# Optimization experiments

Hardware: AMD Instinct MI355X
Metric: run time of the kernel (lower is better)

## Reference

```python
import math
import jax, jax.numpy as jnp
import numpy as np

H = 256      # hidden_size
HEADS = 8
DK = H // HEADS
B = 32
DL = 290     # drug length
PL = 1000    # protein length


def _pe(length, d):
    # sinusoidal positional encoding, d even
    pos = jnp.arange(length, dtype=jnp.float32)[:, None]
    div = jnp.exp(jnp.arange(0, d, 2, dtype=jnp.float32) * (-math.log(10000.0) / d))
    ang = pos * div  # [L, d/2]
    pe = jnp.zeros((length, d), jnp.float32)
    pe = pe.at[:, 0::2].set(jnp.sin(ang)).at[:, 1::2].set(jnp.cos(ang))
    return pe


def setup_inputs() -> dict:
    key = jax.random.key(0)
    ks = iter(jax.random.split(key, 48))
    def lin(din, dout):
        return jax.random.normal(next(ks), (din, dout), jnp.float32) * 0.02, jnp.zeros((dout,), jnp.float32)
    inp = {}
    inp['drug'] = jax.random.normal(next(ks), (B, DL, H), jnp.float32)
    inp['protein'] = jax.random.normal(next(ks), (B, PL, H), jnp.float32)
    inp['scale_d'] = jnp.ones((1,), jnp.float32)
    inp['scale_p'] = jnp.ones((1,), jnp.float32)
    for name in ['q_d', 'k_p', 'v_p', 'q_p', 'k_d', 'v_d', 'out_d', 'out_p']:
        w, b = lin(H, H)
        inp['w_' + name] = w
        inp['b_' + name] = b
    inp['alpha'] = jnp.asarray(0.5, jnp.float32)
    for name in ['fc_dp', 'fc_pd']:
        w, b = lin(HEADS, H)
        inp['w_' + name] = w
        inp['b_' + name] = b
    for name in ['gd', 'gp']:
        w, b = lin(H, H)
        inp['w_' + name] = w
        inp['b_' + name] = b
    return inp


def _split_heads(x):
    b, l, _ = x.shape
    return x.reshape(b, l, HEADS, DK).transpose(0, 2, 1, 3)  # [b, h, l, dk]


def _forward(drug, protein, scale_d, scale_p,
             w_q_d, b_q_d, w_k_p, b_k_p, w_v_p, b_v_p,
             w_q_p, b_q_p, w_k_d, b_k_d, w_v_d, b_v_d,
             alpha, w_out_d, b_out_d, w_out_p, b_out_p,
             w_fc_dp, b_fc_dp, w_fc_pd, b_fc_pd,
             w_gd, b_gd, w_gp, b_gp):
    b, dl, h = drug.shape
    pl = protein.shape[1]
    # positional encoding (buffers, non-learned except scale)
    drug_e = drug + scale_d * _pe(dl, h)
    prot_e = protein + scale_p * _pe(pl, h)

    Qd = _split_heads(drug_e @ w_q_d + b_q_d)   # [b,h,dl,dk]
    Kp = _split_heads(prot_e @ w_k_p + b_k_p)   # [b,h,pl,dk]
    Vp = _split_heads(prot_e @ w_v_p + b_v_p)
    Qp = _split_heads(prot_e @ w_q_p + b_q_p)
    Kd = _split_heads(drug_e @ w_k_d + b_k_d)
    Vd = _split_heads(drug_e @ w_v_d + b_v_d)

    inv_sqrt = 1.0 / math.sqrt(DK)
    attn_dp = jnp.einsum('bhid,bhjd->bhij', Qd, Kp) * inv_sqrt      # [b,h,dl,pl]
    # (Q_p K_d^T)^T along last two dims -> [b,h,dl,pl]
    attn_pd = jnp.einsum('bhjd,bhid->bhij', Qp, Kd) * inv_sqrt
    a = jax.nn.sigmoid(alpha)
    A = jax.nn.softmax(a * attn_dp + (1.0 - a) * attn_pd, axis=-1)  # [b,h,dl,pl]

    ctx_d = jnp.einsum('bhij,bhjd->bhid', A, Vp)  # [b,h,dl,dk]
    ctx_p = jnp.einsum('bhij,bhid->bhjd', A, Vd)  # [b,h,pl,dk]
    ctx_d = ctx_d.transpose(0, 2, 1, 3).reshape(b, dl, h) @ w_out_d + b_out_d
    ctx_p = ctx_p.transpose(0, 2, 1, 3).reshape(b, pl, h) @ w_out_p + b_out_p

    attn_dp_m = jnp.mean(A, axis=-1).transpose(0, 2, 1)   # [b,dl,heads]
    drug_attn = attn_dp_m @ w_fc_dp + b_fc_dp             # [b,dl,h]
    attn_pd_m = jnp.mean(A, axis=-2).transpose(0, 2, 1)   # [b,pl,heads]
    prot_attn = attn_pd_m @ w_fc_pd + b_fc_pd             # [b,pl,h]

    drug_gate = jax.nn.sigmoid(drug_e @ w_gd + b_gd)
    prot_gate = jax.nn.sigmoid(prot_e @ w_gp + b_gp)
    ctx_d = ctx_d * drug_gate
    ctx_p = ctx_p * prot_gate

    drug_upd = drug_e + ctx_d * jax.nn.sigmoid(drug_attn)
    prot_upd = prot_e + ctx_p * jax.nn.sigmoid(prot_attn)
    return jnp.concatenate([drug_upd, prot_upd], axis=1)  # [b, dl+pl, h]


def reference(drug, protein, scale_d, scale_p,
              w_q_d, b_q_d, w_k_p, b_k_p, w_v_p, b_v_p,
              w_q_p, b_q_p, w_k_d, b_k_d, w_v_d, b_v_d,
              alpha, w_out_d, b_out_d, w_out_p, b_out_p,
              w_fc_dp, b_fc_dp, w_fc_pd, b_fc_pd,
              w_gd, b_gd, w_gp, b_gp):
    return _forward(drug, protein, scale_d, scale_p,
                    w_q_d, b_q_d, w_k_p, b_k_p, w_v_p, b_v_p,
                    w_q_p, b_q_p, w_k_d, b_k_d, w_v_d, b_v_d,
                    alpha, w_out_d, b_out_d, w_out_p, b_out_p,
                    w_fc_dp, b_fc_dp, w_fc_pd, b_fc_pd,
                    w_gd, b_gd, w_gp, b_gp)
```

## Files before the change

kernel.cpp:

```cpp
#include <hip/hip_runtime.h>
#include <math.h>

typedef __attribute__((ext_vector_type(8))) short bf16x8;
typedef __attribute__((ext_vector_type(4))) float f32x4;
typedef unsigned short u16;
typedef unsigned int u32;

#define DEVFN static __device__ __forceinline__

constexpr int NB  = 32;
constexpr int DLn = 290;
constexpr int PLc = 1000;
constexpr int MD  = NB * DLn;
constexpr int MP  = NB * PLc;
constexpr int NS2 = 323;
constexpr int SP2 = 73;
constexpr int SG2 = 41;

DEVFN u16 f2b(float f) {
    u32 u = __builtin_bit_cast(u32, f);
    u32 r = u + 0x7fffu + ((u >> 16) & 1u);
    return (u16)(r >> 16);
}
DEVFN u16 f2bh(float f) { __bf16 h = (__bf16)f; return __builtin_bit_cast(u16, h); }
DEVFN float b2f(u16 s) { return __builtin_bit_cast(float, (u32)s << 16); }
DEVFN float sigm(float x) { return 1.0f / (1.0f + __expf(-x)); }
DEVFN float fexp2(float x) { return __builtin_amdgcn_exp2f(x); }
DEVFN int sw(int row, int col, int stride) { return row * stride + (col ^ ((row & 7) << 3)); }

__global__ void pe_kernel(float* __restrict__ pe) {
    int p = blockIdx.x, c = threadIdx.x;
    float div = __expf((float)(c & ~1) * (-9.210340371976184f / 256.0f));
    float ang = (float)p * div;
    pe[p * 256 + c] = (c & 1) ? cosf(ang) : sinf(ang);
}

__global__ void fcprep_kernel(const float* __restrict__ w, const float* __restrict__ b,
                              float* __restrict__ dfc) {
    int c = threadIdx.x;
    float s = b[c];
    #pragma unroll
    for (int hh = 0; hh < 8; hh++) s += 0.001f * w[hh * 256 + c];
    dfc[c] = s;
}

__global__ __launch_bounds__(256) void eadd_kernel(
        const float* __restrict__ drug, const float* __restrict__ prot,
        const float* __restrict__ scale_d, const float* __restrict__ scale_p,
        const float* __restrict__ pe,
        u16* __restrict__ e_d, u16* __restrict__ e_p) {
    int idx = blockIdx.x * 256 + threadIdx.x;
    int r = idx >> 6, c4 = (idx & 63) * 4;
    if (r < MD) {
        int i = r % DLn;
        float s = scale_d[0];
        float4 dv = *(const float4*)&drug[(size_t)r * 256 + c4];
        float4 pv = *(const float4*)&pe[i * 256 + c4];
        u16 o[4];
        o[0] = f2b(dv.x + s * pv.x); o[1] = f2b(dv.y + s * pv.y);
        o[2] = f2b(dv.z + s * pv.z); o[3] = f2b(dv.w + s * pv.w);
        *(uint2*)&e_d[(size_t)r * 256 + c4] = *(uint2*)o;
    } else {
        int rr = r - MD;
        int j = rr % PLc;
        float s = scale_p[0];
        float4 dv = *(const float4*)&prot[(size_t)rr * 256 + c4];
        float4 pv = *(const float4*)&pe[j * 256 + c4];
        u16 o[4];
        o[0] = f2b(dv.x + s * pv.x); o[1] = f2b(dv.y + s * pv.y);
        o[2] = f2b(dv.z + s * pv.z); o[3] = f2b(dv.w + s * pv.w);
        *(uint2*)&e_p[(size_t)rr * 256 + c4] = *(uint2*)o;
    }
}

struct WPtrs { const float* w[10]; };
__global__ __launch_bounds__(256) void wprep_kernel(WPtrs wp, u16* __restrict__ wt) {
    __shared__ u16 t[64][66];
    int m = blockIdx.y, tile = blockIdx.x;
    int k0 = (tile >> 2) * 64, n0 = (tile & 3) * 64;
    const float* w = wp.w[m];
    int r = threadIdx.x >> 6, c = threadIdx.x & 63;
    #pragma unroll
    for (int q = 0; q < 16; q++) {
        int rr = r + q * 4;
        t[rr][c] = f2b(w[(size_t)(k0 + rr) * 256 + n0 + c]);
    }
    __syncthreads();
    #pragma unroll
    for (int q = 0; q < 16; q++) {
        int rr = r + q * 4;
        wt[((size_t)m << 16) + (size_t)(n0 + rr) * 256 + k0 + c] = t[c][rr];
    }
}

struct PM { const u16* BT; const float* bias; u16* C; int sig; };
struct PCfg {
    const u16* Ab;
    PM m[4];
};
struct PCfg2 {
    PCfg c0, c1;
    const float* x0; const float* x1;
    const u16* gate0; const u16* gate1;
    const float* cm;
    const float* dfc;
    const float* wfc1; const float* bfc1;
    const float* scale0; const float* scale1;
    const float* pe;
    float* out;
};

template<int NM>
__global__ __launch_bounds__(512) void proj_kernel(PCfg2 cfgs) {
    const int d = blockIdx.x;
    const int x = d & 7, q = d >> 3;
    const int u  = (NM == 4) ? (q & 15) : (q & 3);
    const int sg = (NM == 4) ? (q >> 4) : (q >> 2);
    const int s = sg * 8 + x;
    if (s >= NS2) return;
    const int mi = (NM == 4) ? (u >> 2) : 0;
    const int nt = (NM == 4) ? (u & 3) : u;
    const bool f1 = s < SP2;
    const int mt = f1 ? s : s - SP2;
    const int Mrows = f1 ? MD : MP;

    const u16* Ab   = f1 ? cfgs.c0.Ab : cfgs.c1.Ab;
    const u16*   BT   = f1 ? (mi==0?cfgs.c0.m[0].BT  :mi==1?cfgs.c0.m[1].BT  :mi==2?cfgs.c0.m[2].BT  :cfgs.c0.m[3].BT)
                           : (mi==0?cfgs.c1.m[0].BT  :mi==1?cfgs.c1.m[1].BT  :mi==2?cfgs.c1.m[2].BT  :cfgs.c1.m[3].BT);
    const float* bias = f1 ? (mi==0?cfgs.c0.m[0].bias:mi==1?cfgs.c0.m[1].bias:mi==2?cfgs.c0.m[2].bias:cfgs.c0.m[3].bias)
                           : (mi==0?cfgs.c1.m[0].bias:mi==1?cfgs.c1.m[1].bias:mi==2?cfgs.c1.m[2].bias:cfgs.c1.m[3].bias);
    u16*         C    = f1 ? (mi==0?cfgs.c0.m[0].C   :mi==1?cfgs.c0.m[1].C   :mi==2?cfgs.c0.m[2].C   :cfgs.c0.m[3].C)
                           : (mi==0?cfgs.c1.m[0].C   :mi==1?cfgs.c1.m[1].C   :mi==2?cfgs.c1.m[2].C   :cfgs.c1.m[3].C);
    const int    sig  = f1 ? (mi==0?cfgs.c0.m[0].sig :mi==1?cfgs.c0.m[1].sig :mi==2?cfgs.c0.m[2].sig :cfgs.c0.m[3].sig)
                           : (mi==0?cfgs.c1.m[0].sig :mi==1?cfgs.c1.m[1].sig :mi==2?cfgs.c1.m[2].sig :cfgs.c1.m[3].sig);

    __shared__ u16 Bs[64 * 256];
    __shared__ float fcb[(NM == 1) ? 2304 : 4];
    const int tid = threadIdx.x;
    const int lane = tid & 63, w = tid >> 6, ln = lane & 15, g = lane >> 4;

    const int gc = tid & 31;
    const int rb = (tid >> 5) * 4;
    uint4 bv[4];
    #pragma unroll
    for (int kk = 0; kk < 4; kk++) {
        const int r = rb + kk;
        const int nur = ((r >> 5) & 1) * 32 + ((r >> 2) & 3) * 8 + ((r >> 4) & 1) * 4 + (r & 3);
        bv[kk] = *(const uint4*)(BT + (size_t)(nt * 64 + nur) * 256 + gc * 8);
    }

    const int row = mt * 128 + w * 16 + ln;
    const bool rowok = row < Mrows;
    bf16x8 Af[8];
    if (rowok) {
        const u16* Ap = Ab + (size_t)row * 256 + g * 8;
        #pragma unroll
        for (int ks = 0; ks < 8; ks++)
            Af[ks] = *(const bf16x8*)(Ap + ks * 32);
    } else {
        u16 z[8] = {0,0,0,0,0,0,0,0};
        #pragma unroll
        for (int ks = 0; ks < 8; ks++) Af[ks] = *(bf16x8*)z;
    }

    if (NM == 1 && !f1 && tid < 256) {
        *(float4*)&fcb[tid * 8]     = *(const float4*)&cfgs.wfc1[tid * 8];
        *(float4*)&fcb[tid * 8 + 4] = *(const float4*)&cfgs.wfc1[tid * 8 + 4];
        fcb[2048 + tid] = cfgs.bfc1[tid];
    }

    #pragma unroll
    for (int kk = 0; kk < 4; kk++) {
        const int r = rb + kk;
        *(uint4*)&Bs[sw(r, gc * 8, 256)] = bv[kk];
    }
    __syncthreads();

    f32x4 acc[4] = {};
    #pragma unroll
    for (int ks = 0; ks < 8; ks++) {
        #pragma unroll
        for (int ntl = 0; ntl < 4; ntl++) {
            bf16x8 bf = *(const bf16x8*)&Bs[sw(ntl * 16 + ln, ks * 32 + g * 8, 256)];
            acc[ntl] = __builtin_amdgcn_mfma_f32_16x16x32_bf16(bf, Af[ks], acc[ntl], 0, 0, 0);
        }
    }

    const int base0 = nt * 64 + g * 8, base1 = base0 + 32;
    f32x4 b0 = *(const f32x4*)&bias[base0];
    f32x4 b1 = *(const f32x4*)&bias[base0 + 4];
    f32x4 b2 = *(const f32x4*)&bias[base1];
    f32x4 b3 = *(const f32x4*)&bias[base1 + 4];
    float v[16];
    #pragma unroll
    for (int t = 0; t < 4; t++) {
        v[t]      = acc[0][t] + b0[t];
        v[4 + t]  = acc[1][t] + b1[t];
        v[8 + t]  = acc[2][t] + b2[t];
        v[12 + t] = acc[3][t] + b3[t];
    }
    if (NM == 4) {
        if (rowok) {
            if (sig) {
                #pragma unroll
                for (int t = 0; t < 16; t++) v[t] = sigm(v[t]);
            }
            u16 o[16];
            #pragma unroll
            for (int t = 0; t < 16; t++) o[t] = f2b(v[t]);
            u16* Cp = C + (size_t)row * 256;
            *(uint4*)&Cp[base0] = *(uint4*)&o[0];
            *(uint4*)&Cp[base1] = *(uint4*)&o[8];
        }
    } else if (rowok) {
        (void)C; (void)sig;
        const float* X     = f1 ? cfgs.x0 : cfgs.x1;
        const u16* gate    = f1 ? cfgs.gate0 : cfgs.gate1;
        const float* scale = f1 ? cfgs.scale0 : cfgs.scale1;
        const float* pe    = cfgs.pe;
        const float sc = scale[0];
        const int pos  = f1 ? (row % DLn) : (row % PLc);
        const int bidx = f1 ? (row / DLn) : (row / PLc);
        const int orow = bidx * 1290 + (f1 ? pos : 290 + pos);
        float aw[16];
        if (f1) {
            const float* dfc = cfgs.dfc;
            *(float4*)&aw[0]  = *(const float4*)&dfc[base0];
            *(float4*)&aw[4]  = *(const float4*)&dfc[base0 + 4];
            *(float4*)&aw[8]  = *(const float4*)&dfc[base1];
            *(float4*)&aw[12] = *(const float4*)&dfc[base1 + 4];
        } else {
            float cmv[8];
            float4 ca = *(const float4*)&cfgs.cm[(size_t)row * 8];
            float4 cb = *(const float4*)&cfgs.cm[(size_t)row * 8 + 4];
            cmv[0]=ca.x; cmv[1]=ca.y; cmv[2]=ca.z; cmv[3]=ca.w;
            cmv[4]=cb.x; cmv[5]=cb.y; cmv[6]=cb.z; cmv[7]=cb.w;
            #pragma unroll
            for (int t = 0; t < 16; t++) {
                const int col = (t < 8) ? (base0 + t) : (base1 + t - 8);
                float s2 = fcb[2048 + col];
                #pragma unroll
                for (int hh = 0; hh < 8; hh++) s2 += cmv[hh] * fcb[hh * 256 + col];
                aw[t] = s2;
            }
        }
        u16 ge[16];
        *(uint4*)&ge[0] = *(const uint4*)&gate[(size_t)row * 256 + base0];
        *(uint4*)&ge[8] = *(const uint4*)&gate[(size_t)row * 256 + base1];
        float outv[16];
        #pragma unroll
        for (int half = 0; half < 2; half++) {
            const int cb0 = half ? base1 : base0;
            #pragma unroll
            for (int t4 = 0; t4 < 2; t4++) {
                float4 xa = *(const float4*)&X[(size_t)row * 256 + cb0 + t4 * 4];
                float4 pa = *(const float4*)&pe[(size_t)pos * 256 + cb0 + t4 * 4];
                #pragma unroll
                for (int t = 0; t < 4; t++) {
                    const int idx = half * 8 + t4 * 4 + t;
                    float e = (&xa.x)[t] + sc * (&pa.x)[t];
                    outv[idx] = e + v[idx] * b2f(ge[idx]) * sigm(aw[idx]);
                }
            }
        }
        float* Op = cfgs.out + (size_t)orow * 256;
        *(float4*)&Op[base0]     = *(float4*)&outv[0];
        *(float4*)&Op[base0 + 4] = *(float4*)&outv[4];
        *(float4*)&Op[base1]     = *(float4*)&outv[8];
        *(float4*)&Op[base1 + 4] = *(float4*)&outv[12];
    }
}

__global__ __launch_bounds__(512) void attn_kernel(
        const u16* __restrict__ Qd, const u16* __restrict__ Kd, const u16* __restrict__ Vd,
        const u16* __restrict__ Kp, const u16* __restrict__ Vp, const u16* __restrict__ Qp,
        const float* __restrict__ alpha,
        u16* __restrict__ ctx_d, u16* __restrict__ ctx_p, float* __restrict__ cm) {
    __shared__ u16 Ks[2][64 * 64];
    __shared__ union {
        struct { u16 VpT[2][32 * 64]; u16 Pm[320 * 64]; } s1;
        struct { u16 PT[64 * 320]; u16 VdT[32 * 320]; } s2;
    } U;
    __shared__ float r_l[320];
    __shared__ float colpart[8][64];

    const int bh = blockIdx.x, b = bh >> 3, h = bh & 7;
    const int tid = threadIdx.x;
    const int w = tid >> 6, lane = tid & 63, ln = lane & 15, g = lane >> 4;

    const float a = sigm(alpha[0]);
    const float inv = 0.1767766952966369f;
    const float l2e = 1.4426950408889634f;
    const float sa = a * inv * l2e, sb = (1.0f - a) * inv * l2e;
    const int nmt = (w < 4) ? 3 : 2;
    const int mtsA[3] = { w, w + 8, w + 16 };

    const size_t rbd = (size_t)b * DLn * 256 + h * 32;
    const size_t rbp = (size_t)b * PLc * 256 + h * 32;

    bf16x8 Qf[3][2];
    #pragma unroll
    for (int t = 0; t < 3; t++) {
        const int i = mtsA[t] * 16 + ln;
        #pragma unroll
        for (int ks = 0; ks < 2; ks++) {
            u16 o[8] = {0,0,0,0,0,0,0,0};
            if (t < nmt && i < DLn) {
                const u16* src = (ks ? Kd : Qd) + rbd + (size_t)i * 256 + g * 8;
                const float s = ks ? sb : sa;
                uint4 v = *(const uint4*)src;
                u16 e[8]; *(uint4*)e = v;
                #pragma unroll
                for (int q = 0; q < 8; q++) o[q] = f2bh(b2f(e[q]) * s);
            }
            Qf[t][ks] = *(bf16x8*)o;
        }
    }

    const int s_jj = tid >> 3, s_ch = tid & 7;
    const u16* s_src = ((s_ch >> 2) ? Qp : Kp) + rbp + (s_ch & 3) * 8;
    const int v_j = tid & 63, v_d0 = (tid >> 6) * 4;

    {
        int j = s_jj;
        uint4 kv = (j < PLc) ? *(const uint4*)(s_src + (size_t)j * 256) : make_uint4(0,0,0,0);
        uint2 vv = (v_j < PLc) ? *(const uint2*)(Vp + rbp + (size_t)v_j * 256 + v_d0) : make_uint2(0,0);
        *(uint4*)&Ks[0][sw(s_jj, s_ch * 8, 64)] = kv;
        u16 e[4]; *(uint2*)e = vv;
        #pragma unroll
        for (int q = 0; q < 4; q++) U.s1.VpT[0][sw(v_d0 + q, v_j, 64)] = e[q];
    }
    __syncthreads();

    float rs[3] = {0.f, 0.f, 0.f};
    f32x4 accd[3][2] = {};
    for (int jt = 0; jt < 16; jt++) {
        const int cur = jt & 1, j0 = jt * 64;
        const int jn = j0 + 64 + s_jj;
        uint4 kv = (jn < PLc) ? *(const uint4*)(s_src + (size_t)jn * 256) : make_uint4(0,0,0,0);
        const int vn = j0 + 64 + v_j;
        uint2 vv = (vn < PLc) ? *(const uint2*)(Vp + rbp + (size_t)vn * 256 + v_d0) : make_uint2(0,0);

        bf16x8 kf[4][2];
        #pragma unroll
        for (int js = 0; js < 4; js++)
            #pragma unroll
            for (int ks = 0; ks < 2; ks++)
                kf[js][ks] = *(const bf16x8*)&Ks[cur][sw(js * 16 + ln, ks * 32 + g * 8, 64)];

        #pragma unroll
        for (int t = 0; t < 3; t++) {
            if (t >= nmt) break;
            const int mt = mtsA[t];
            f32x4 acc[4] = {};
            #pragma unroll
            for (int ks = 0; ks < 2; ks++)
                #pragma unroll
                for (int js = 0; js < 4; js++)
                    acc[js] = __builtin_amdgcn_mfma_f32_16x16x32_bf16(kf[js][ks], Qf[t][ks], acc[js], 0, 0, 0);
            const int irow = mt * 16 + ln;
            #pragma unroll
            for (int js = 0; js < 4; js++) {
                u16 pb[4];
                float psum = 0.f;
                #pragma unroll
                for (int r = 0; r < 4; r++) {
                    float p = fexp2(acc[js][r]);
                    psum += p;
                    pb[r] = f2bh(p);
                }
                rs[t] += psum;
                *(ushort4*)&U.s1.Pm[sw(irow, js * 16 + g * 4, 64)] = *(ushort4*)pb;
            }
        }
        #pragma unroll
        for (int t = 0; t < 3; t++) {
            if (t >= nmt) break;
            const int mt = mtsA[t];
            #pragma unroll
            for (int ks2 = 0; ks2 < 2; ks2++) {
                bf16x8 af = *(const bf16x8*)&U.s1.Pm[sw(mt * 16 + ln, ks2 * 32 + g * 8, 64)];
                #pragma unroll
                for (int nd = 0; nd < 2; nd++) {
                    bf16x8 bv = *(const bf16x8*)&U.s1.VpT[cur][sw(nd * 16 + ln, ks2 * 32 + g * 8, 64)];
                    accd[t][nd] = __builtin_amdgcn_mfma_f32_16x16x32_bf16(bv, af, accd[t][nd], 0, 0, 0);
                }
            }
        }
        *(uint4*)&Ks[cur ^ 1][sw(s_jj, s_ch * 8, 64)] = kv;
        {
            u16 e[4]; *(uint2*)e = vv;
            #pragma unroll
            for (int q = 0; q < 4; q++) U.s1.VpT[cur ^ 1][sw(v_d0 + q, v_j, 64)] = e[q];
        }
        __syncthreads();
    }

    #pragma unroll
    for (int t = 0; t < 3; t++) {
        float v = rs[t];
        v += __shfl_xor(v, 16);
        v += __shfl_xor(v, 32);
        rs[t] = v;
    }
    if (g == 0) {
        #pragma unroll
        for (int t = 0; t < 3; t++) {
            if (t >= nmt) break;
            const int i = mtsA[t] * 16 + ln;
            r_l[i] = (i < DLn) ? 1.0f / (rs[t] - 24.0f) : 0.0f;
        }
    }
    __syncthreads();

    #pragma unroll
    for (int t = 0; t < 3; t++) {
        if (t >= nmt) break;
        const int i = mtsA[t] * 16 + ln;
        if (i < DLn) {
            const float ri = r_l[i];
            #pragma unroll
            for (int nd = 0; nd < 2; nd++) {
                u16 o[4];
                #pragma unroll
                for (int r = 0; r < 4; r++) o[r] = f2bh(accd[t][nd][r] * ri);
                *(uint2*)&ctx_d[rbd + (size_t)i * 256 + nd * 16 + g * 4] = *(uint2*)o;
            }
        }
    }
    for (int c = tid; c < 320 * 8; c += 512) {
        const int i = c >> 3, d0 = (c & 7) * 4;
        u16 o[4] = {0,0,0,0};
        if (i < DLn) {
            const float ri = r_l[i];
            uint2 v = *(const uint2*)(Vd + rbd + (size_t)i * 256 + d0);
            u16 e[4]; *(uint2*)e = v;
            #pragma unroll
            for (int q = 0; q < 4; q++) o[q] = f2bh(b2f(e[q]) * ri);
        }
        #pragma unroll
        for (int q = 0; q < 4; q++) U.s2.VdT[sw(d0 + q, i, 320)] = o[q];
    }
    {
        int j = s_jj;
        uint4 kv = (j < PLc) ? *(const uint4*)(s_src + (size_t)j * 256) : make_uint4(0,0,0,0);
        *(uint4*)&Ks[0][sw(s_jj, s_ch * 8, 64)] = kv;
    }
    float rr[3][4];
    #pragma unroll
    for (int t = 0; t < 3; t++)
        #pragma unroll
        for (int r = 0; r < 4; r++)
            rr[t][r] = (t < nmt) ? r_l[mtsA[t] * 16 + g * 4 + r] : 0.0f;
    __syncthreads();

    for (int jt = 0; jt < 16; jt++) {
        const int cur = jt & 1, j0 = jt * 64;
        const int jn = j0 + 64 + s_jj;
        uint4 kv = (jn < PLc) ? *(const uint4*)(s_src + (size_t)jn * 256) : make_uint4(0,0,0,0);

        bf16x8 kf[4][2];
        #pragma unroll
        for (int js = 0; js < 4; js++)
            #pragma unroll
            for (int ks = 0; ks < 2; ks++)
                kf[js][ks] = *(const bf16x8*)&Ks[cur][sw(js * 16 + ln, ks * 32 + g * 8, 64)];

        float csl[4] = {0.f, 0.f, 0.f, 0.f};
        #pragma unroll
        for (int t = 0; t < 3; t++) {
            if (t >= nmt) break;
            const int mt = mtsA[t];
            f32x4 acc[4] = {};
            #pragma unroll
            for (int ks = 0; ks < 2; ks++)
                #pragma unroll
                for (int js = 0; js < 4; js++)
                    acc[js] = __builtin_amdgcn_mfma_f32_16x16x32_bf16(Qf[t][ks], kf[js][ks], acc[js], 0, 0, 0);
            #pragma unroll
            for (int js = 0; js < 4; js++) {
                u16 pb[4];
                #pragma unroll
                for (int r = 0; r < 4; r++) {
                    float p = fexp2(acc[js][r]);
                    csl[js] += p * rr[t][r];
                    pb[r] = f2bh(p);
                }
                *(ushort4*)&U.s2.PT[sw(js * 16 + ln, mt * 16 + g * 4, 320)] = *(ushort4*)pb;
            }
        }
        #pragma unroll
        for (int js = 0; js < 4; js++) {
            float v = csl[js];
            v += __shfl_xor(v, 16);
            v += __shfl_xor(v, 32);
            csl[js] = v;
        }
        if (g == 0) {
            #pragma unroll
            for (int js = 0; js < 4; js++) colpart[w][js * 16 + ln] = csl[js];
        }
        *(uint4*)&Ks[cur ^ 1][sw(s_jj, s_ch * 8, 64)] = kv;
        __syncthreads();

        {
            const int js2 = w & 3, ds2 = w >> 2;
            f32x4 ap = {};
            #pragma unroll
            for (int k = 0; k < 10; k++) {
                bf16x8 af = *(const bf16x8*)&U.s2.PT[sw(js2 * 16 + ln, k * 32 + g * 8, 320)];
                bf16x8 bv = *(const bf16x8*)&U.s2.VdT[sw(ds2 * 16 + ln, k * 32 + g * 8, 320)];
                ap = __builtin_amdgcn_mfma_f32_16x16x32_bf16(bv, af, ap, 0, 0, 0);
            }
            const int j = j0 + js2 * 16 + ln;
            if (j < PLc) {
                u16 o[4];
                #pragma unroll
                for (int r = 0; r < 4; r++) o[r] = f2bh(ap[r]);
                *(uint2*)&ctx_p[rbp + (size_t)j * 256 + ds2 * 16 + g * 4] = *(uint2*)o;
            }
        }
        if (w == 0) {
            float tot = 0.f;
            #pragma unroll
            for (int ww = 0; ww < 8; ww++) tot += colpart[ww][lane];
            const int j = j0 + lane;
            if (j < PLc) cm[(size_t)(b * PLc + j) * 8 + h] = tot * (1.0f / 290.0f);
        }
        __syncthreads();
    }
}

extern "C" void kernel_launch(void* const* d_in, const int* in_sizes, int n_in,
                              void* d_out, int out_size, void* d_ws, size_t ws_size,
                              hipStream_t stream) {
    (void)in_sizes; (void)n_in; (void)out_size;
    const float* drug    = (const float*)d_in[0];
    const float* prot    = (const float*)d_in[1];
    const float* scale_d = (const float*)d_in[2];
    const float* scale_p = (const float*)d_in[3];

    char* ws = (char*)d_ws;
    size_t off = 0;
    auto alloc = [&](size_t bytes) -> void* {
        void* p = ws + off;
        off += (bytes + 255) & ~(size_t)255;
        return p;
    };
    float* pe   = (float*)alloc((size_t)1000 * 256 * 4);
    u16* wt     = (u16*)alloc((size_t)10 * 65536 * 2);
    u16* e_d    = (u16*)alloc((size_t)MD * 256 * 2);
    u16* e_p    = (u16*)alloc((size_t)MP * 256 * 2);
    u16* Qd     = (u16*)alloc((size_t)MD * 256 * 2);
    u16* Kd     = (u16*)alloc((size_t)MD * 256 * 2);
    u16* Vd     = (u16*)alloc((size_t)MD * 256 * 2);
    u16* gate_d = (u16*)alloc((size_t)MD * 256 * 2);
    u16* Kp     = (u16*)alloc((size_t)MP * 256 * 2);
    u16* Vp     = (u16*)alloc((size_t)MP * 256 * 2);
    u16* Qp     = (u16*)alloc((size_t)MP * 256 * 2);
    u16* gate_p = (u16*)alloc((size_t)MP * 256 * 2);
    u16* ctxd   = (u16*)alloc((size_t)MD * 256 * 2);
    u16* ctxp   = (u16*)alloc((size_t)MP * 256 * 2);
    float* cm   = (float*)alloc((size_t)MP * 8 * 4);
    float* dfc  = (float*)alloc((size_t)256 * 4);
    if (off > ws_size) return;

    pe_kernel<<<1000, 256, 0, stream>>>(pe);
    fcprep_kernel<<<1, 256, 0, stream>>>((const float*)d_in[21], (const float*)d_in[22], dfc);

    WPtrs wp;
    const int wsrc[10] = {4, 12, 14, 25, 6, 8, 10, 27, 16, 18};
    for (int m = 0; m < 10; m++) wp.w[m] = (const float*)d_in[wsrc[m]];
    wprep_kernel<<<dim3(16, 10), 256, 0, stream>>>(wp, wt);

    eadd_kernel<<<(MD + MP) / 4, 256, 0, stream>>>(drug, prot, scale_d, scale_p, pe, e_d, e_p);

    auto W = [&](int slot) { return wt + (size_t)slot * 65536; };

    PCfg2 p1 = {};
    p1.c0 = { e_d,
              { { W(0), (const float*)d_in[5],  Qd,     0 },
                { W(1), (const float*)d_in[13], Kd,     0 },
                { W(2), (const float*)d_in[15], Vd,     0 },
                { W(3), (const float*)d_in[26], gate_d, 1 } } };
    p1.c1 = { e_p,
              { { W(4), (const float*)d_in[7],  Kp,     0 },
                { W(5), (const float*)d_in[9],  Vp,     0 },
                { W(6), (const float*)d_in[11], Qp,     0 },
                { W(7), (const float*)d_in[28], gate_p, 1 } } };
    proj_kernel<4><<<SG2 * 8 * 16, 512, 0, stream>>>(p1);

    attn_kernel<<<256, 512, 0, stream>>>(Qd, Kd, Vd, Kp, Vp, Qp,
                                         (const float*)d_in[20], ctxd, ctxp, cm);

    PCfg2 p2 = {};
    p2.c0 = { ctxd, { { W(8), (const float*)d_in[17], nullptr, 0 }, {}, {}, {} } };
    p2.c1 = { ctxp, { { W(9), (const float*)d_in[19], nullptr, 0 }, {}, {}, {} } };
    p2.x0 = drug;  p2.x1 = prot;
    p2.gate0 = gate_d;  p2.gate1 = gate_p;
    p2.cm = cm;
    p2.dfc = dfc;
    p2.wfc1 = (const float*)d_in[23];  p2.bfc1 = (const float*)d_in[24];
    p2.scale0 = scale_d;  p2.scale1 = scale_p;
    p2.pe = pe;
    p2.out = (float*)d_out;
    proj_kernel<1><<<SG2 * 8 * 4, 512, 0, stream>>>(p2);
}
```

Baseline: 174.9 us.

## Stage K/Q tiles via direct global-to-LDS loads and simplify bf16 rounding

Replaces the register-staged K/Q tile loads in the attention kernel with global_load_lds async copies into swizzled LDS slots. Rows past the sequence end are read from zero-padded extra rows appended to Kp/Qp, and a new zfill kernel clears those rows. Masking of out-of-range columns in the row sums replaces the fixed -24 correction. It also swaps the manual bf16 rounding for the hardware conversion. The aim is to free VGPRs and issue slots used to stage K, at the cost of an extra launch and reliance on the LDS address layout matching the swizzle.

New measurement: 189.6 us. 1.08x slower.

```diff
diff --git a/kernel.cpp b/kernel.cpp
--- a/kernel.cpp
+++ b/kernel.cpp
@@ -17,11 +17,6 @@
 constexpr int SP2 = 73;
 constexpr int SG2 = 41;
 
-DEVFN u16 f2b(float f) {
-    u32 u = __builtin_bit_cast(u32, f);
-    u32 r = u + 0x7fffu + ((u >> 16) & 1u);
-    return (u16)(r >> 16);
-}
 DEVFN u16 f2bh(float f) { __bf16 h = (__bf16)f; return __builtin_bit_cast(u16, h); }
 DEVFN float b2f(u16 s) { return __builtin_bit_cast(float, (u32)s << 16); }
 DEVFN float sigm(float x) { return 1.0f / (1.0f + __expf(-x)); }
@@ -33,6 +28,12 @@
     float div = __expf((float)(c & ~1) * (-9.210340371976184f / 256.0f));
     float ang = (float)p * div;
     pe[p * 256 + c] = (c & 1) ? cosf(ang) : sinf(ang);
+}
+
+__global__ void zfill_kernel(u16* __restrict__ a, u16* __restrict__ b) {
+    int i = blockIdx.x * 256 + threadIdx.x;
+    a[i] = 0;
+    b[i] = 0;
 }
 
 __global__ void fcprep_kernel(const float* __restrict__ w, const float* __restrict__ b,
@@ -57,8 +58,8 @@
         float4 dv = *(const float4*)&drug[(size_t)r * 256 + c4];
         float4 pv = *(const float4*)&pe[i * 256 + c4];
         u16 o[4];
-        o[0] = f2b(dv.x + s * pv.x); o[1] = f2b(dv.y + s * pv.y);
-        o[2] = f2b(dv.z + s * pv.z); o[3] = f2b(dv.w + s * pv.w);
+        o[0] = f2bh(dv.x + s * pv.x); o[1] = f2bh(dv.y + s * pv.y);
+        o[2] = f2bh(dv.z + s * pv.z); o[3] = f2bh(dv.w + s * pv.w);
         *(uint2*)&e_d[(size_t)r * 256 + c4] = *(uint2*)o;
     } else {
         int rr = r - MD;
@@ -67,8 +68,8 @@
         float4 dv = *(const float4*)&prot[(size_t)rr * 256 + c4];
         float4 pv = *(const float4*)&pe[j * 256 + c4];
         u16 o[4];
-        o[0] = f2b(dv.x + s * pv.x); o[1] = f2b(dv.y + s * pv.y);
-        o[2] = f2b(dv.z + s * pv.z); o[3] = f2b(dv.w + s * pv.w);
+        o[0] = f2bh(dv.x + s * pv.x); o[1] = f2bh(dv.y + s * pv.y);
+        o[2] = f2bh(dv.z + s * pv.z); o[3] = f2bh(dv.w + s * pv.w);
         *(uint2*)&e_p[(size_t)rr * 256 + c4] = *(uint2*)o;
     }
 }
@@ -83,7 +84,7 @@
     #pragma unroll
     for (int q = 0; q < 16; q++) {
         int rr = r + q * 4;
-        t[rr][c] = f2b(w[(size_t)(k0 + rr) * 256 + n0 + c]);
+        t[rr][c] = f2bh(w[(size_t)(k0 + rr) * 256 + n0 + c]);
     }
     __syncthreads();
     #pragma unroll
@@ -207,7 +208,7 @@
             }
             u16 o[16];
             #pragma unroll
-            for (int t = 0; t < 16; t++) o[t] = f2b(v[t]);
+            for (int t = 0; t < 16; t++) o[t] = f2bh(v[t]);
             u16* Cp = C + (size_t)row * 256;
             *(uint4*)&Cp[base0] = *(uint4*)&o[0];
             *(uint4*)&Cp[base1] = *(uint4*)&o[8];
@@ -317,15 +318,25 @@
         }
     }
 
-    const int s_jj = tid >> 3, s_ch = tid & 7;
-    const u16* s_src = ((s_ch >> 2) ? Qp : Kp) + rbp + (s_ch & 3) * 8;
+    const int wvu = __builtin_amdgcn_readfirstlane(tid >> 6);
+    const int kr  = lane >> 3;
+    const int kgr = lane & 7;
+    const int ksg = kgr ^ kr;
+    const int krow = wvu * 8 + kr;
+    const u16* kp_src = ((ksg < 4) ? Kp : Qp) + rbp + (size_t)krow * 256 + (ksg & 3) * 8;
+    #define STAGE_K(buf, j0) do { \
+        u16* _dst = &Ks[buf][0] + (wvu << 9); \
+        const u16* _src = kp_src + (size_t)(j0) * 256; \
+        __builtin_amdgcn_global_load_lds( \
+            (const __attribute__((address_space(1))) void*)_src, \
+            (__attribute__((address_space(3))) void*)_dst, 16, 0, 0); \
+    } while (0)
+
     const int v_j = tid & 63, v_d0 = (tid >> 6) * 4;
 
+    STAGE_K(0, 0);
     {
-        int j = s_jj;
-        uint4 kv = (j < PLc) ? *(const uint4*)(s_src + (size_t)j * 256) : make_uint4(0,0,0,0);
         uint2 vv = (v_j < PLc) ? *(const uint2*)(Vp + rbp + (size_t)v_j * 256 + v_d0) : make_uint2(0,0);
-        *(uint4*)&Ks[0][sw(s_jj, s_ch * 8, 64)] = kv;
         u16 e[4]; *(uint2*)e = vv;
         #pragma unroll
         for (int q = 0; q < 4; q++) U.s1.VpT[0][sw(v_d0 + q, v_j, 64)] = e[q];
@@ -336,8 +347,8 @@
     f32x4 accd[3][2] = {};
     for (int jt = 0; jt < 16; jt++) {
         const int cur = jt & 1, j0 = jt * 64;
-        const int jn = j0 + 64 + s_jj;
-        uint4 kv = (jn < PLc) ? *(const uint4*)(s_src + (size_t)jn * 256) : make_uint4(0,0,0,0);
+        const bool lastT = (jt == 15);
+        if (!lastT) STAGE_K(cur ^ 1, j0 + 64);
         const int vn = j0 + 64 + v_j;
         uint2 vv = (vn < PLc) ? *(const uint2*)(Vp + rbp + (size_t)vn * 256 + v_d0) : make_uint2(0,0);
 
@@ -366,7 +377,7 @@
                 #pragma unroll
                 for (int r = 0; r < 4; r++) {
                     float p = fexp2(acc[js][r]);
-                    psum += p;
+                    if (!lastT || (j0 + js * 16 + g * 4 + r) < PLc) psum += p;
                     pb[r] = f2bh(p);
                 }
                 rs[t] += psum;
@@ -387,7 +398,6 @@
                 }
             }
         }
-        *(uint4*)&Ks[cur ^ 1][sw(s_jj, s_ch * 8, 64)] = kv;
         {
             u16 e[4]; *(uint2*)e = vv;
             #pragma unroll
@@ -408,7 +418,7 @@
         for (int t = 0; t < 3; t++) {
             if (t >= nmt) break;
             const int i = mtsA[t] * 16 + ln;
-            r_l[i] = (i < DLn) ? 1.0f / (rs[t] - 24.0f) : 0.0f;
+            r_l[i] = (i < DLn) ? 1.0f / rs[t] : 0.0f;
         }
     }
     __syncthreads();
@@ -441,11 +451,7 @@
         #pragma unroll
         for (int q = 0; q < 4; q++) U.s2.VdT[sw(d0 + q, i, 320)] = o[q];
     }
-    {
-        int j = s_jj;
-        uint4 kv = (j < PLc) ? *(const uint4*)(s_src + (size_t)j * 256) : make_uint4(0,0,0,0);
-        *(uint4*)&Ks[0][sw(s_jj, s_ch * 8, 64)] = kv;
-    }
+    STAGE_K(0, 0);
     float rr[3][4];
     #pragma unroll
     for (int t = 0; t < 3; t++)
@@ -456,8 +462,7 @@
 
     for (int jt = 0; jt < 16; jt++) {
         const int cur = jt & 1, j0 = jt * 64;
-        const int jn = j0 + 64 + s_jj;
-        uint4 kv = (jn < PLc) ? *(const uint4*)(s_src + (size_t)jn * 256) : make_uint4(0,0,0,0);
+        if (jt < 15) STAGE_K(cur ^ 1, j0 + 64);
 
         bf16x8 kf[4][2];
         #pragma unroll
@@ -500,7 +505,6 @@
             #pragma unroll
             for (int js = 0; js < 4; js++) colpart[w][js * 16 + ln] = csl[js];
         }
-        *(uint4*)&Ks[cur ^ 1][sw(s_jj, s_ch * 8, 64)] = kv;
         __syncthreads();
 
         {
@@ -529,6 +533,7 @@
         }
         __syncthreads();
     }
+    #undef STAGE_K
 }
 
 extern "C" void kernel_launch(void* const* d_in, const int* in_sizes, int n_in,
@@ -555,9 +560,9 @@
     u16* Kd     = (u16*)alloc((size_t)MD * 256 * 2);
     u16* Vd     = (u16*)alloc((size_t)MD * 256 * 2);
     u16* gate_d = (u16*)alloc((size_t)MD * 256 * 2);
-    u16* Kp     = (u16*)alloc((size_t)MP * 256 * 2);
+    u16* Kp     = (u16*)alloc((size_t)(MP + 24) * 256 * 2);
     u16* Vp     = (u16*)alloc((size_t)MP * 256 * 2);
-    u16* Qp     = (u16*)alloc((size_t)MP * 256 * 2);
+    u16* Qp     = (u16*)alloc((size_t)(MP + 24) * 256 * 2);
     u16* gate_p = (u16*)alloc((size_t)MP * 256 * 2);
     u16* ctxd   = (u16*)alloc((size_t)MD * 256 * 2);
     u16* ctxp   = (u16*)alloc((size_t)MP * 256 * 2);
@@ -566,6 +571,7 @@
     if (off > ws_size) return;
 
     pe_kernel<<<1000, 256, 0, stream>>>(pe);
+    zfill_kernel<<<24, 256, 0, stream>>>(Kp + (size_t)MP * 256, Qp + (size_t)MP * 256);
     fcprep_kernel<<<1, 256, 0, stream>>>((const float*)d_in[21], (const float*)d_in[22], dfc);
 
     WPtrs wp;
```
